# Optimization experiments

Hardware: AMD Instinct MI355X
Metric: run time of the kernel (lower is better)

The kernel has to match this reference:

```python
import jax, jax.numpy as jnp
import numpy as np

H = 1024
NUM_HEADS = 16
E = 4
I = H * 4 // E  # expert intermediate size = 1024
EPS = 1e-6


def layer_norm(x, g, b):
    mu = jnp.mean(x, axis=-1, keepdims=True)
    var = jnp.mean(jnp.square(x - mu), axis=-1, keepdims=True)
    return (x - mu) * jax.lax.rsqrt(var + EPS) * g + b


def setup_inputs() -> dict:
    key = jax.random.key(0)
    ks = jax.random.split(key, 12)
    B, Nq, Nkv = 4, 1024, 2048
    inp = {
        "query": jax.random.normal(ks[0], (B, Nq, H), jnp.float32),
        "key_value": jax.random.normal(ks[1], (B, Nkv, H), jnp.float32),
        "Wq": jax.random.normal(ks[2], (H, H), jnp.float32) * 0.02,
        "bq": jnp.zeros((H,), jnp.float32),
        "Wk": jax.random.normal(ks[3], (H, H), jnp.float32) * 0.02,
        "bk": jnp.zeros((H,), jnp.float32),
        "Wv": jax.random.normal(ks[4], (H, H), jnp.float32) * 0.02,
        "bv": jnp.zeros((H,), jnp.float32),
        "Wo": jax.random.normal(ks[5], (H, H), jnp.float32) * 0.02,
        "bo": jnp.zeros((H,), jnp.float32),
        "g1": jnp.ones((H,), jnp.float32),
        "b1": jnp.zeros((H,), jnp.float32),
        "g2": jnp.ones((H,), jnp.float32),
        "b2": jnp.zeros((H,), jnp.float32),
        "gate_up": jax.random.normal(ks[6], (E, H, 2 * I), jnp.float32) * 0.02,
        "down": jax.random.normal(ks[7], (E, I, H), jnp.float32) * 0.02,
    }
    return inp


def reference(query, key_value, Wq, bq, Wk, bk, Wv, bv, Wo, bo,
              g1, b1, g2, b2, gate_up, down):
    B, Nq, _ = query.shape
    Nkv = key_value.shape[1]
    d = H // NUM_HEADS
    scale = d ** -0.5

    # ---- cross-attention with pre-norm + residual ----
    x = layer_norm(query, g1, b1)
    q = (x @ Wq + bq).reshape(B, Nq, NUM_HEADS, d)
    k = (key_value @ Wk + bk).reshape(B, Nkv, NUM_HEADS, d)
    v = (key_value @ Wv + bv).reshape(B, Nkv, NUM_HEADS, d)
    scores = jnp.einsum("bqhd,bkhd->bhqk", q, k) * scale
    attn = jax.nn.softmax(scores, axis=-1)
    ctx = jnp.einsum("bhqk,bkhd->bqhd", attn, v).reshape(B, Nq, H)
    x = query + (ctx @ Wo + bo)

    # ---- token-routed MoE SwiGLU MLP (expert = pos % E) ----
    residual = x
    h = layer_norm(x, g2, b2)
    outs = []
    for e in range(E):
        xe = h[:, e::E]                      # [B, Nq/E, H] tokens routed to expert e
        gu = xe @ gate_up[e]                 # [B, Nq/E, 2I]
        gate, up = gu[..., :I], gu[..., I:]
        inter = jax.nn.silu(gate) * up
        outs.append(inter @ down[e])         # [B, Nq/E, H]
    moe = jnp.stack(outs, axis=2).reshape(B, Nq, H)  # interleave back to position order
    return residual + moe
```

## Files before the change

kernel.cpp:

```cpp
#include <hip/hip_runtime.h>
#include <hip/hip_bf16.h>

typedef unsigned short u16;
typedef float f32x4 __attribute__((ext_vector_type(4)));
typedef short s16x8 __attribute__((ext_vector_type(8)));

__device__ __forceinline__ u16 f2b(float f) {
    union { float f; unsigned u; } c; c.f = f;
    unsigned r = c.u + 0x7fffu + ((c.u >> 16) & 1u);
    return (u16)(r >> 16);
}
__device__ __forceinline__ unsigned pkbf16(float a, float b) {
    union { __hip_bfloat162 h; unsigned u; } c;
    c.h = __float22bfloat162_rn(float2{a, b});
    return c.u;
}

#define ASYNC_COPY16(gp, lp)                                                       \
    __builtin_amdgcn_global_load_lds(                                              \
        (const __attribute__((address_space(1))) void*)(gp),                       \
        (__attribute__((address_space(3))) void*)(lp), 16, 0, 0)

__device__ __forceinline__ void transcast_body(const float* __restrict__ Wz,
                                               u16* __restrict__ Wtz,
                                               int K, int N, int bx, int by,
                                               int permute) {
    __shared__ float tile[64][65];
    const int n0 = bx * 64, k0 = by * 64;
    const int tid = threadIdx.x;
    const int tx = tid & 15, ty = tid >> 4;
#pragma unroll
    for (int it = 0; it < 4; it++) {
        int r = ty + it * 16;
        float4 v = *(const float4*)&Wz[(size_t)(k0 + r) * N + n0 + tx * 4];
        tile[r][tx * 4 + 0] = v.x;
        tile[r][tx * 4 + 1] = v.y;
        tile[r][tx * 4 + 2] = v.z;
        tile[r][tx * 4 + 3] = v.w;
    }
    __syncthreads();
    int n = tid >> 2;
    int ks = (tid & 3) * 16;
    int drow = n0 + n;
    if (permute) drow = (drow < 1024) ? 2 * drow : 2 * (drow - 1024) + 1;
    u16* dst = &Wtz[(size_t)drow * K + k0 + ks];
#pragma unroll
    for (int h = 0; h < 2; h++) {
        uint4 o;
        o.x = pkbf16(tile[ks + h * 8 + 0][n], tile[ks + h * 8 + 1][n]);
        o.y = pkbf16(tile[ks + h * 8 + 2][n], tile[ks + h * 8 + 3][n]);
        o.z = pkbf16(tile[ks + h * 8 + 4][n], tile[ks + h * 8 + 5][n]);
        o.w = pkbf16(tile[ks + h * 8 + 6][n], tile[ks + h * 8 + 7][n]);
        *(uint4*)(dst + h * 8) = o;
    }
}

__global__ __launch_bounds__(256) void transcast64(const float* __restrict__ W,
                                                   u16* __restrict__ Wt,
                                                   int K, int N, long long zstride,
                                                   int permute) {
    transcast_body(W + (size_t)blockIdx.z * zstride, Wt + (size_t)blockIdx.z * zstride,
                   K, N, blockIdx.x, blockIdx.y, permute);
}

__global__ __launch_bounds__(256) void transcast4(
    const float* __restrict__ W0, const float* __restrict__ W1,
    const float* __restrict__ W2, const float* __restrict__ W3,
    u16* __restrict__ O0, u16* __restrict__ O1,
    u16* __restrict__ O2, u16* __restrict__ O3) {
    const int z = blockIdx.z;
    const float* W = (z == 0) ? W0 : (z == 1) ? W1 : (z == 2) ? W2 : W3;
    u16* O = (z == 0) ? O0 : (z == 1) ? O1 : (z == 2) ? O2 : O3;
    transcast_body(W, O, 1024, 1024, blockIdx.x, blockIdx.y, 0);
}

__global__ __launch_bounds__(256) void cast_kernel(const float* __restrict__ x,
                                                   u16* __restrict__ y, int n8) {
    int id = blockIdx.x * 256 + threadIdx.x;
    if (id >= n8) return;
    const float* p = x + (size_t)id * 8;
    float4 a = *(const float4*)p;
    float4 b = *(const float4*)(p + 4);
    uint4 o;
    o.x = pkbf16(a.x, a.y);
    o.y = pkbf16(a.z, a.w);
    o.z = pkbf16(b.x, b.y);
    o.w = pkbf16(b.z, b.w);
    *(uint4*)(y + (size_t)id * 8) = o;
}

__global__ __launch_bounds__(256) void ln_kernel(const float* __restrict__ x,
                                                 const float* __restrict__ g,
                                                 const float* __restrict__ bb,
                                                 u16* __restrict__ out, int pack) {
    int token = blockIdx.x;
    int tid = threadIdx.x;
    const float* row = x + (size_t)token * 1024;
    float4 v = *(const float4*)(row + tid * 4);
    float s1 = v.x + v.y + v.z + v.w;
    float s2 = v.x * v.x + v.y * v.y + v.z * v.z + v.w * v.w;
#pragma unroll
    for (int off = 32; off > 0; off >>= 1) {
        s1 += __shfl_down(s1, off);
        s2 += __shfl_down(s2, off);
    }
    __shared__ float ws1[4], ws2[4];
    int wave = tid >> 6;
    if ((tid & 63) == 0) { ws1[wave] = s1; ws2[wave] = s2; }
    __syncthreads();
    float t1 = ws1[0] + ws1[1] + ws1[2] + ws1[3];
    float t2 = ws2[0] + ws2[1] + ws2[2] + ws2[3];
    float mean = t1 * (1.f / 1024.f);
    float var = t2 * (1.f / 1024.f) - mean * mean;
    float rstd = rsqrtf(var + 1e-6f);
    size_t dest = token;
    if (pack) {
        int bq = token >> 10, q = token & 1023;
        dest = (size_t)(q & 3) * 1024 + (size_t)bq * 256 + (q >> 2);
    }
    int c = tid * 4;
    float4 gv = *(const float4*)(g + c);
    float4 bv = *(const float4*)(bb + c);
    uint2 o;
    o.x = pkbf16((v.x - mean) * rstd * gv.x + bv.x, (v.y - mean) * rstd * gv.y + bv.y);
    o.y = pkbf16((v.z - mean) * rstd * gv.z + bv.z, (v.w - mean) * rstd * gv.w + bv.w);
    *(uint2*)&out[dest * 1024 + c] = o;
}

template <int BM>
__global__ __launch_bounds__(256) void gemm_t(
    const u16* __restrict__ A, const u16* __restrict__ Bt,
    const float* __restrict__ bias0, const float* __restrict__ bias1, int biasSplit,
    const float* __restrict__ resid,
    float* __restrict__ outF, u16* __restrict__ outH, u16* __restrict__ outH2,
    int M, int N, int K,
    long long aStride, long long bStride, long long oStride,
    int mode, float outScale) {
    constexpr int NJ = (BM == 128) ? 4 : 2;
    __shared__ __align__(16) u16 As[BM * 64];
    __shared__ __align__(16) u16 Bs[128 * 64];
    const int z = blockIdx.z;
    const u16* Ab = A + (size_t)z * aStride;
    const u16* Bb = Bt + (size_t)z * bStride;
    const int m0 = blockIdx.y * BM, n0 = blockIdx.x * 128;
    const int tid = threadIdx.x;
    const int wave = tid >> 6, lane = tid & 63;
    const int wm = (BM == 128) ? (wave >> 1) * 64 : 0;
    const int wn = (BM == 128) ? (wave & 1) * 64 : wave * 32;
    const int quad = lane >> 4, l16 = lane & 15;
    f32x4 acc[4][NJ] = {};
    for (int k0 = 0; k0 < K; k0 += 64) {
#pragma unroll
        for (int i = 0; i < BM / 32; i++) {
            int id = tid + i * 256;
            int row = id >> 3, c = id & 7;
            int srcseg = c ^ (row & 7);
            ASYNC_COPY16(&Ab[(size_t)(m0 + row) * K + k0 + srcseg * 8],
                         As + (size_t)(wave * 64 + i * 256) * 8);
        }
#pragma unroll
        for (int i = 0; i < 4; i++) {
            int id = tid + i * 256;
            int row = id >> 3, c = id & 7;
            int srcseg = c ^ (row & 7);
            ASYNC_COPY16(&Bb[(size_t)(n0 + row) * K + k0 + srcseg * 8],
                         Bs + (size_t)(wave * 64 + i * 256) * 8);
        }
        __syncthreads();
#pragma unroll
        for (int kk = 0; kk < 2; kk++) {
            s16x8 af[4], bfr[NJ];
#pragma unroll
            for (int i = 0; i < 4; i++) {
                int row = wm + i * 16 + l16;
                af[i] = *(const s16x8*)&As[row * 64 + ((kk * 4 + quad) ^ (row & 7)) * 8];
            }
#pragma unroll
            for (int j = 0; j < NJ; j++) {
                int row = wn + j * 16 + l16;
                bfr[j] = *(const s16x8*)&Bs[row * 64 + ((kk * 4 + quad) ^ (row & 7)) * 8];
            }
#pragma unroll
            for (int i = 0; i < 4; i++)
#pragma unroll
                for (int j = 0; j < NJ; j++)
                    acc[i][j] = __builtin_amdgcn_mfma_f32_16x16x32_bf16(af[i], bfr[j], acc[i][j], 0, 0, 0);
        }
        __syncthreads();
    }
#pragma unroll
    for (int i = 0; i < 4; i++) {
#pragma unroll
        for (int j = 0; j < NJ; j++) {
            int col = n0 + wn + j * 16 + l16;
            float bv = 0.f;
            if (bias0) bv = (col < biasSplit) ? bias0[col] : bias1[col - biasSplit];
            if (mode == 3) {
                float vr[4];
#pragma unroll
                for (int r = 0; r < 4; r++) vr[r] = acc[i][j][r] + bv;
                int row0 = m0 + wm + i * 16 + quad * 4;
                if (col < 1024) {
#pragma unroll
                    for (int r = 0; r < 4; r++)
                        outH[(size_t)(row0 + r) * 1024 + col] = f2b(vr[r]);
                } else {
                    int bb2 = row0 >> 11, key = row0 & 2047;
                    int hh = (col - 1024) >> 6, d = (col - 1024) & 63;
                    uint2 dw;
                    dw.x = pkbf16(vr[0], vr[1]);
                    dw.y = pkbf16(vr[2], vr[3]);
                    *(uint2*)&outH2[(((size_t)bb2 * 16 + hh) * 64 + d) * 2048 + key] = dw;
                }
                continue;
            }
#pragma unroll
            for (int r = 0; r < 4; r++) {
                int row = m0 + wm + i * 16 + quad * 4 + r;
                float v = acc[i][j][r] + bv;
                if (mode == 2) {
                    float other = __shfl_xor(v, 1);
                    if (!(lane & 1)) {
                        float res = (v / (1.f + __expf(-v))) * other;
                        outH[(size_t)z * oStride + (size_t)row * (N >> 1) + (col >> 1)] = f2b(res);
                    }
                } else if (mode == 1) {
                    int bb2 = row >> 8, qi = row & 255;
                    size_t oidx = ((size_t)bb2 * 1024 + (size_t)z + 4 * (size_t)qi) * N + col;
                    outF[oidx] = v + resid[oidx];
                } else {
                    size_t oidx = (size_t)z * oStride + (size_t)row * N + col;
                    if (resid) v += resid[oidx];
                    if (outF) outF[oidx] = v;
                    else outH[oidx] = f2b(v * outScale);
                }
            }
        }
    }
}

__global__ __launch_bounds__(256) void flash_attn(
    const u16* __restrict__ Q, const u16* __restrict__ Kb,
    const u16* __restrict__ VT, u16* __restrict__ O) {
    const int lidx = blockIdx.x;
    const int xcd = lidx & 7, slot = lidx >> 3;
    const int g = xcd + 8 * (slot >> 4);
    const int qt = slot & 15;
    const int b = g >> 4, h = g & 15;
    const int tid = threadIdx.x, wave = tid >> 6, lane = tid & 63;
    const int quad = lane >> 4, l16 = lane & 15;
    const int q0 = qt * 64 + wave * 16;

    __shared__ __align__(16) u16 Ks[64 * 64];
    __shared__ __align__(16) u16 Vs[64 * 64];
    __shared__ __align__(16) unsigned Pt[4][16 * 36];

    const size_t qrow = ((size_t)b * 1024 + q0 + l16) * 1024 + (size_t)h * 64;
    s16x8 qf0 = *(const s16x8*)&Q[qrow + quad * 8];
    s16x8 qf1 = *(const s16x8*)&Q[qrow + 32 + quad * 8];

    f32x4 o[4] = {};
    float l = 0.f;
    const float C2 = 5.770780163555852f;

    const u16* Kbh = Kb + ((size_t)b * 2048) * 1024 + (size_t)h * 64;
    const u16* VTbh = VT + (((size_t)b * 16 + h) * 64) * 2048;
    const uint4* Ks128 = (const uint4*)Ks;
    const uint4* Vs128 = (const uint4*)Vs;

    for (int kc = 0; kc < 2048; kc += 64) {
        __syncthreads();
#pragma unroll
        for (int i = 0; i < 2; i++) {
            int id = tid + i * 256;
            int row = id >> 3;
            int srcseg = (id & 7) ^ (row & 7);
            ASYNC_COPY16(Kbh + (size_t)(kc + row) * 1024 + srcseg * 8,
                         &Ks[(size_t)(wave * 64 + i * 256) * 8]);
        }
#pragma unroll
        for (int i = 0; i < 2; i++) {
            int id = tid + i * 256;
            int row = id >> 3;
            int srcseg = (id & 7) ^ (row & 7);
            ASYNC_COPY16(VTbh + (size_t)row * 2048 + kc + srcseg * 8,
                         &Vs[(size_t)(wave * 64 + i * 256) * 8]);
        }
        __syncthreads();

        f32x4 s[4];
#pragma unroll
        for (int kt = 0; kt < 4; kt++) {
            int row = kt * 16 + l16;
            union { uint4 v; s16x8 f; } a0, a1;
            a0.v = Ks128[row * 8 + (quad ^ (row & 7))];
            a1.v = Ks128[row * 8 + ((4 + quad) ^ (row & 7))];
            f32x4 acc = {};
            acc = __builtin_amdgcn_mfma_f32_16x16x32_bf16(a0.f, qf0, acc, 0, 0, 0);
            acc = __builtin_amdgcn_mfma_f32_16x16x32_bf16(a1.f, qf1, acc, 0, 0, 0);
            s[kt] = acc;
        }

        float p[16], rs = 0.f;
#pragma unroll
        for (int kt = 0; kt < 4; kt++)
#pragma unroll
            for (int r = 0; r < 4; r++) {
                float e = exp2f(s[kt][r] - C2);
                p[kt * 4 + r] = e;
                rs += e;
            }
        rs += __shfl_xor(rs, 16);
        rs += __shfl_xor(rs, 32);
        l += rs;

        unsigned* pw = &Pt[wave][l16 * 36];
#pragma unroll
        for (int kt = 0; kt < 4; kt++) {
            uint2 dw;
            dw.x = pkbf16(p[kt * 4 + 0], p[kt * 4 + 1]);
            dw.y = pkbf16(p[kt * 4 + 2], p[kt * 4 + 3]);
            *(uint2*)&pw[kt * 8 + quad * 2] = dw;
        }
        asm volatile("s_waitcnt lgkmcnt(0)" ::: "memory");

#pragma unroll
        for (int c = 0; c < 2; c++) {
            union { uint4 v; s16x8 f; } pf;
            pf.v = *(const uint4*)&Pt[wave][l16 * 36 + c * 16 + quad * 4];
#pragma unroll
            for (int dt = 0; dt < 4; dt++) {
                int row = dt * 16 + l16;
                union { uint4 v; s16x8 f; } vf;
                vf.v = Vs128[row * 8 + ((c * 4 + quad) ^ (row & 7))];
                o[dt] = __builtin_amdgcn_mfma_f32_16x16x32_bf16(vf.f, pf.f, o[dt], 0, 0, 0);
            }
        }
    }

    float inv = 1.f / l;
    size_t orow = ((size_t)b * 1024 + q0 + l16) * 1024 + (size_t)h * 64;
#pragma unroll
    for (int dt = 0; dt < 4; dt++) {
        uint2 dw;
        dw.x = pkbf16(o[dt][0] * inv, o[dt][1] * inv);
        dw.y = pkbf16(o[dt][2] * inv, o[dt][3] * inv);
        *(uint2*)&O[orow + dt * 16 + quad * 4] = dw;
    }
}

extern "C" void kernel_launch(void* const* d_in, const int* in_sizes, int n_in,
                              void* d_out, int out_size, void* d_ws, size_t ws_size,
                              hipStream_t stream) {
    (void)in_sizes; (void)n_in; (void)out_size; (void)ws_size;
    const float* query     = (const float*)d_in[0];
    const float* key_value = (const float*)d_in[1];
    const float* Wq = (const float*)d_in[2];
    const float* bq = (const float*)d_in[3];
    const float* Wk = (const float*)d_in[4];
    const float* bk = (const float*)d_in[5];
    const float* Wv = (const float*)d_in[6];
    const float* bv = (const float*)d_in[7];
    const float* Wo = (const float*)d_in[8];
    const float* bo = (const float*)d_in[9];
    const float* g1 = (const float*)d_in[10];
    const float* b1 = (const float*)d_in[11];
    const float* g2 = (const float*)d_in[12];
    const float* b2 = (const float*)d_in[13];
    const float* gate_up = (const float*)d_in[14];
    const float* down    = (const float*)d_in[15];
    float* out = (float*)d_out;

    char* wsb = (char*)d_ws;
    size_t off = 0;
    auto alloc = [&](size_t bytes) {
        char* p = wsb + off;
        off += (bytes + 255) & ~(size_t)255;
        return (void*)p;
    };
    u16* buf8a = (u16*)alloc((size_t)4096 * 1024 * 2);
    u16* qb    = (u16*)alloc((size_t)4096 * 1024 * 2);
    u16* kvb   = (u16*)alloc((size_t)8192 * 1024 * 2);
    u16* vtb   = (u16*)alloc((size_t)8192 * 1024 * 2);
    u16* kvbf  = (u16*)alloc((size_t)8192 * 1024 * 2);
    float* x2  = (float*)alloc((size_t)4096 * 1024 * 4);
    u16* wqt   = (u16*)alloc((size_t)1024 * 1024 * 2);
    u16* kvw   = (u16*)alloc((size_t)2048 * 1024 * 2);
    u16* wot   = (u16*)alloc((size_t)1024 * 1024 * 2);
    u16* gut   = (u16*)alloc((size_t)4 * 2048 * 1024 * 2);
    u16* dnt   = (u16*)alloc((size_t)4 * 1024 * 1024 * 2);
    u16* xn = buf8a; u16* ctx = buf8a; u16* hp = buf8a;
    u16* inter = kvbf;
    const int BIG = 1 << 30;
    const float QSCALE = 0.125f * 1.44269504f;

    transcast4<<<dim3(16, 16, 4), 256, 0, stream>>>(
        Wq, Wk, Wv, Wo, wqt, kvw, kvw + (size_t)1024 * 1024, wot);
    transcast64<<<dim3(32, 16, 4), 256, 0, stream>>>(gate_up, gut, 1024, 2048, (long long)1024 * 2048, 1);
    transcast64<<<dim3(16, 16, 4), 256, 0, stream>>>(down, dnt, 1024, 1024, (long long)1024 * 1024, 0);
    cast_kernel<<<4096, 256, 0, stream>>>(key_value, kvbf, 1048576);
    ln_kernel<<<4096, 256, 0, stream>>>(query, g1, b1, xn, 0);
    gemm_t<64><<<dim3(8, 64, 1), 256, 0, stream>>>(xn, wqt, bq, bq, BIG, nullptr, nullptr, qb, nullptr,
        4096, 1024, 1024, 0, 0, 0, 0, QSCALE);
    gemm_t<128><<<dim3(16, 64, 1), 256, 0, stream>>>(kvbf, kvw, bk, bv, 1024, nullptr, nullptr, kvb, vtb,
        8192, 2048, 1024, 0, 0, 0, 3, 1.f);
    flash_attn<<<1024, 256, 0, stream>>>(qb, kvb, vtb, ctx);
    gemm_t<64><<<dim3(8, 64, 1), 256, 0, stream>>>(ctx, wot, bo, bo, BIG, query, x2, nullptr, nullptr,
        4096, 1024, 1024, 0, 0, 0, 0, 1.f);
    ln_kernel<<<4096, 256, 0, stream>>>(x2, g2, b2, hp, 1);
    gemm_t<64><<<dim3(16, 16, 4), 256, 0, stream>>>(hp, gut, nullptr, nullptr, BIG, nullptr, nullptr, inter, nullptr,
        1024, 2048, 1024,
        (long long)1024 * 1024, (long long)2048 * 1024, (long long)1024 * 1024, 2, 1.f);
    gemm_t<64><<<dim3(8, 16, 4), 256, 0, stream>>>(inter, dnt, nullptr, nullptr, BIG, x2, out, nullptr, nullptr,
        1024, 1024, 1024,
        (long long)1024 * 1024, (long long)1024 * 1024, 0, 1, 1.f);
}
```

Measured before the change: 423.4 us.

## Process two query tiles per wave and 128-key chunks in flash attention

Each attention block now handles 128 queries, with every wave computing two 16-row query tiles, and stages 128 keys per iteration instead of 64. Each K/V fragment loaded from LDS is reused for two MFMA chains, and the number of K/V global loads and barriers per output is halved. The cost is higher register pressure, larger LDS use, a wider swizzle for V, and half as many blocks (512), which may reduce occupancy and latency hiding.

```diff
diff --git a/kernel.cpp b/kernel.cpp
--- a/kernel.cpp
+++ b/kernel.cpp
@@ -244,23 +244,26 @@
     const u16* __restrict__ VT, u16* __restrict__ O) {
     const int lidx = blockIdx.x;
     const int xcd = lidx & 7, slot = lidx >> 3;
-    const int g = xcd + 8 * (slot >> 4);
-    const int qt = slot & 15;
+    const int g = xcd + 8 * (slot >> 3);
+    const int qblk = slot & 7;
     const int b = g >> 4, h = g & 15;
     const int tid = threadIdx.x, wave = tid >> 6, lane = tid & 63;
     const int quad = lane >> 4, l16 = lane & 15;
-    const int q0 = qt * 64 + wave * 16;
-
-    __shared__ __align__(16) u16 Ks[64 * 64];
-    __shared__ __align__(16) u16 Vs[64 * 64];
-    __shared__ __align__(16) unsigned Pt[4][16 * 36];
-
-    const size_t qrow = ((size_t)b * 1024 + q0 + l16) * 1024 + (size_t)h * 64;
-    s16x8 qf0 = *(const s16x8*)&Q[qrow + quad * 8];
-    s16x8 qf1 = *(const s16x8*)&Q[qrow + 32 + quad * 8];
-
-    f32x4 o[4] = {};
-    float l = 0.f;
+    const int q0 = qblk * 128 + wave * 16;
+
+    __shared__ __align__(16) u16 Ks[128 * 64];
+    __shared__ __align__(16) u16 Vs[64 * 128];
+    __shared__ __align__(16) unsigned Pt[4][2][16 * 34];
+
+    const size_t qrowA = ((size_t)b * 1024 + q0 + l16) * 1024 + (size_t)h * 64;
+    const size_t qrowB = qrowA + (size_t)64 * 1024;
+    s16x8 qA0 = *(const s16x8*)&Q[qrowA + quad * 8];
+    s16x8 qA1 = *(const s16x8*)&Q[qrowA + 32 + quad * 8];
+    s16x8 qB0 = *(const s16x8*)&Q[qrowB + quad * 8];
+    s16x8 qB1 = *(const s16x8*)&Q[qrowB + 32 + quad * 8];
+
+    f32x4 o0[4] = {}, o1[4] = {};
+    float l0 = 0.f, l1 = 0.f;
     const float C2 = 5.770780163555852f;
 
     const u16* Kbh = Kb + ((size_t)b * 2048) * 1024 + (size_t)h * 64;
@@ -268,84 +271,96 @@
     const uint4* Ks128 = (const uint4*)Ks;
     const uint4* Vs128 = (const uint4*)Vs;
 
-    for (int kc = 0; kc < 2048; kc += 64) {
+    for (int kc = 0; kc < 2048; kc += 128) {
         __syncthreads();
 #pragma unroll
-        for (int i = 0; i < 2; i++) {
+        for (int i = 0; i < 4; i++) {
             int id = tid + i * 256;
-            int row = id >> 3;
-            int srcseg = (id & 7) ^ (row & 7);
-            ASYNC_COPY16(Kbh + (size_t)(kc + row) * 1024 + srcseg * 8,
-                         &Ks[(size_t)(wave * 64 + i * 256) * 8]);
-        }
-#pragma unroll
-        for (int i = 0; i < 2; i++) {
+            int row = id >> 3, c = id & 7;
+            ASYNC_COPY16(Kbh + (size_t)(kc + row) * 1024 + (size_t)(c ^ (row & 7)) * 8,
+                         Ks + (size_t)(wave * 64 + i * 256) * 8);
+        }
+#pragma unroll
+        for (int i = 0; i < 4; i++) {
             int id = tid + i * 256;
-            int row = id >> 3;
-            int srcseg = (id & 7) ^ (row & 7);
-            ASYNC_COPY16(VTbh + (size_t)row * 2048 + kc + srcseg * 8,
-                         &Vs[(size_t)(wave * 64 + i * 256) * 8]);
+            int row = id >> 4, c = id & 15;
+            ASYNC_COPY16(VTbh + (size_t)row * 2048 + kc + (size_t)(c ^ (row & 15)) * 8,
+                         Vs + (size_t)(wave * 64 + i * 256) * 8);
         }
         __syncthreads();
 
-        f32x4 s[4];
-#pragma unroll
-        for (int kt = 0; kt < 4; kt++) {
-            int row = kt * 16 + l16;
-            union { uint4 v; s16x8 f; } a0, a1;
-            a0.v = Ks128[row * 8 + (quad ^ (row & 7))];
-            a1.v = Ks128[row * 8 + ((4 + quad) ^ (row & 7))];
-            f32x4 acc = {};
-            acc = __builtin_amdgcn_mfma_f32_16x16x32_bf16(a0.f, qf0, acc, 0, 0, 0);
-            acc = __builtin_amdgcn_mfma_f32_16x16x32_bf16(a1.f, qf1, acc, 0, 0, 0);
-            s[kt] = acc;
-        }
-
-        float p[16], rs = 0.f;
-#pragma unroll
-        for (int kt = 0; kt < 4; kt++)
-#pragma unroll
-            for (int r = 0; r < 4; r++) {
-                float e = exp2f(s[kt][r] - C2);
-                p[kt * 4 + r] = e;
-                rs += e;
-            }
-        rs += __shfl_xor(rs, 16);
-        rs += __shfl_xor(rs, 32);
-        l += rs;
-
-        unsigned* pw = &Pt[wave][l16 * 36];
-#pragma unroll
-        for (int kt = 0; kt < 4; kt++) {
-            uint2 dw;
-            dw.x = pkbf16(p[kt * 4 + 0], p[kt * 4 + 1]);
-            dw.y = pkbf16(p[kt * 4 + 2], p[kt * 4 + 3]);
-            *(uint2*)&pw[kt * 8 + quad * 2] = dw;
-        }
-        asm volatile("s_waitcnt lgkmcnt(0)" ::: "memory");
-
-#pragma unroll
-        for (int c = 0; c < 2; c++) {
-            union { uint4 v; s16x8 f; } pf;
-            pf.v = *(const uint4*)&Pt[wave][l16 * 36 + c * 16 + quad * 4];
-#pragma unroll
-            for (int dt = 0; dt < 4; dt++) {
-                int row = dt * 16 + l16;
-                union { uint4 v; s16x8 f; } vf;
-                vf.v = Vs128[row * 8 + ((c * 4 + quad) ^ (row & 7))];
-                o[dt] = __builtin_amdgcn_mfma_f32_16x16x32_bf16(vf.f, pf.f, o[dt], 0, 0, 0);
-            }
-        }
-    }
-
-    float inv = 1.f / l;
-    size_t orow = ((size_t)b * 1024 + q0 + l16) * 1024 + (size_t)h * 64;
+#pragma unroll
+        for (int h2 = 0; h2 < 2; h2++) {
+            f32x4 s0[4], s1[4];
+#pragma unroll
+            for (int kt = 0; kt < 4; kt++) {
+                int row = h2 * 64 + kt * 16 + l16;
+                union { uint4 v; s16x8 f; } a0, a1;
+                a0.v = Ks128[row * 8 + (quad ^ (row & 7))];
+                a1.v = Ks128[row * 8 + ((4 + quad) ^ (row & 7))];
+                f32x4 t0 = {}, t1 = {};
+                t0 = __builtin_amdgcn_mfma_f32_16x16x32_bf16(a0.f, qA0, t0, 0, 0, 0);
+                t0 = __builtin_amdgcn_mfma_f32_16x16x32_bf16(a1.f, qA1, t0, 0, 0, 0);
+                t1 = __builtin_amdgcn_mfma_f32_16x16x32_bf16(a0.f, qB0, t1, 0, 0, 0);
+                t1 = __builtin_amdgcn_mfma_f32_16x16x32_bf16(a1.f, qB1, t1, 0, 0, 0);
+                s0[kt] = t0; s1[kt] = t1;
+            }
+            float rs0 = 0.f, rs1 = 0.f;
+            float p0[16], p1[16];
+#pragma unroll
+            for (int kt = 0; kt < 4; kt++)
+#pragma unroll
+                for (int r = 0; r < 4; r++) {
+                    float e0 = exp2f(s0[kt][r] - C2);
+                    float e1 = exp2f(s1[kt][r] - C2);
+                    p0[kt * 4 + r] = e0; rs0 += e0;
+                    p1[kt * 4 + r] = e1; rs1 += e1;
+                }
+            rs0 += __shfl_xor(rs0, 16); rs0 += __shfl_xor(rs0, 32);
+            rs1 += __shfl_xor(rs1, 16); rs1 += __shfl_xor(rs1, 32);
+            l0 += rs0; l1 += rs1;
+            unsigned* pw0 = &Pt[wave][0][l16 * 34];
+            unsigned* pw1 = &Pt[wave][1][l16 * 34];
+#pragma unroll
+            for (int kt = 0; kt < 4; kt++) {
+                uint2 d0, d1;
+                d0.x = pkbf16(p0[kt * 4 + 0], p0[kt * 4 + 1]);
+                d0.y = pkbf16(p0[kt * 4 + 2], p0[kt * 4 + 3]);
+                d1.x = pkbf16(p1[kt * 4 + 0], p1[kt * 4 + 1]);
+                d1.y = pkbf16(p1[kt * 4 + 2], p1[kt * 4 + 3]);
+                *(uint2*)&pw0[kt * 8 + quad * 2] = d0;
+                *(uint2*)&pw1[kt * 8 + quad * 2] = d1;
+            }
+            asm volatile("s_waitcnt lgkmcnt(0)" ::: "memory");
+#pragma unroll
+            for (int c2 = 0; c2 < 2; c2++) {
+                union { uint4 v; s16x8 f; } pf0, pf1;
+                pf0.v = *(const uint4*)&Pt[wave][0][l16 * 34 + c2 * 16 + quad * 4];
+                pf1.v = *(const uint4*)&Pt[wave][1][l16 * 34 + c2 * 16 + quad * 4];
+#pragma unroll
+                for (int dt = 0; dt < 4; dt++) {
+                    int row = dt * 16 + l16;
+                    union { uint4 v; s16x8 f; } vf;
+                    vf.v = Vs128[row * 16 + ((h2 * 8 + c2 * 4 + quad) ^ (row & 15))];
+                    o0[dt] = __builtin_amdgcn_mfma_f32_16x16x32_bf16(vf.f, pf0.f, o0[dt], 0, 0, 0);
+                    o1[dt] = __builtin_amdgcn_mfma_f32_16x16x32_bf16(vf.f, pf1.f, o1[dt], 0, 0, 0);
+                }
+            }
+        }
+    }
+
+    float i0 = 1.f / l0, i1 = 1.f / l1;
+    size_t orowA = ((size_t)b * 1024 + q0 + l16) * 1024 + (size_t)h * 64;
+    size_t orowB = orowA + (size_t)64 * 1024;
 #pragma unroll
     for (int dt = 0; dt < 4; dt++) {
-        uint2 dw;
-        dw.x = pkbf16(o[dt][0] * inv, o[dt][1] * inv);
-        dw.y = pkbf16(o[dt][2] * inv, o[dt][3] * inv);
-        *(uint2*)&O[orow + dt * 16 + quad * 4] = dw;
+        uint2 dA, dB;
+        dA.x = pkbf16(o0[dt][0] * i0, o0[dt][1] * i0);
+        dA.y = pkbf16(o0[dt][2] * i0, o0[dt][3] * i0);
+        dB.x = pkbf16(o1[dt][0] * i1, o1[dt][1] * i1);
+        dB.y = pkbf16(o1[dt][2] * i1, o1[dt][3] * i1);
+        *(uint2*)&O[orowA + dt * 16 + quad * 4] = dA;
+        *(uint2*)&O[orowB + dt * 16 + quad * 4] = dB;
     }
 }
 
@@ -404,7 +419,7 @@
         4096, 1024, 1024, 0, 0, 0, 0, QSCALE);
     gemm_t<128><<<dim3(16, 64, 1), 256, 0, stream>>>(kvbf, kvw, bk, bv, 1024, nullptr, nullptr, kvb, vtb,
         8192, 2048, 1024, 0, 0, 0, 3, 1.f);
-    flash_attn<<<1024, 256, 0, stream>>>(qb, kvb, vtb, ctx);
+    flash_attn<<<512, 256, 0, stream>>>(qb, kvb, vtb, ctx);
     gemm_t<64><<<dim3(8, 64, 1), 256, 0, stream>>>(ctx, wot, bo, bo, BIG, query, x2, nullptr, nullptr,
         4096, 1024, 1024, 0, 0, 0, 0, 1.f);
     ln_kernel<<<4096, 256, 0, stream>>>(x2, g2, b2, hp, 1);
```

Measured after the change: 431.7 us. No clear change (+2.0%).
